# Performance work log

Hardware: AMD Instinct MI355X
Metric: run time of the kernel (lower is better)

The kernel has to match this reference:

```python
import jax, jax.numpy as jnp
import numpy as np

N_NODES = 50000
N_EDGES = 1600000
D = 64  # in_features == out_features (required by residual index_add)
N_NBR_FEA = 41


def setup_inputs() -> dict:
    key = jax.random.key(0)
    k1, k2, k3, k4, k5 = jax.random.split(key, 5)
    return {
        "x": jax.random.normal(k1, (N_NODES, D), dtype=jnp.float32),
        # torch Linear(in=D, out=2D, bias=False): weight shape [2D, D]
        "W": jax.random.normal(k2, (2 * D, D), dtype=jnp.float32) * (1.0 / np.sqrt(D)),
        "edge_sources": jax.random.randint(k3, (N_EDGES,), 0, N_NODES),
        "edge_targets": jax.random.randint(k4, (N_EDGES,), 0, N_NODES),
        # required forward arg; unused when use_distance_nbr=False
        "distance_nbr": jax.random.normal(k5, (N_EDGES, N_NBR_FEA), dtype=jnp.float32),
    }


def reference(x, W, edge_sources, edge_targets, distance_nbr):
    # gather neighbor (target) node features per edge: [E, D]
    h = x[edge_targets]
    # edge linear -> gate + message halves: [E, 2D]
    ge = h @ W.T
    g, e = jnp.split(ge, 2, axis=1)
    msg = jax.nn.sigmoid(g) * e  # gate_activation = Sigmoid(); edge/node activations are None
    # output = input.clone(); output.index_add_(0, edge_sources, g * e)
    return x.at[edge_sources].add(msg)
```

## Files before the change

### kernel.cpp

```cpp
#include <hip/hip_runtime.h>

#define NDIM 64
#define WPAD 68
#define BINSHIFT 8
#define BINSZ 256
#define LCAP 12288
#define EPT 16
#define PCHUNK (256 * EPT)

typedef unsigned short ushort;

__device__ __forceinline__ ushort f2bf(float f) {
    unsigned u = __float_as_uint(f);
    return (ushort)((u + 0x7FFFu + ((u >> 16) & 1u)) >> 16);
}
__device__ __forceinline__ float bflo(unsigned u) { return __uint_as_float(u << 16); }
__device__ __forceinline__ float bfhi(unsigned u) { return __uint_as_float(u & 0xFFFF0000u); }

__global__ __launch_bounds__(256) void node_msg_kernel(
    const float* __restrict__ x, const float* __restrict__ W,
    ushort* __restrict__ Mb, int n_nodes)
{
    __shared__ float sW[128 * WPAD];
    __shared__ float sx[4][4][64];

    for (int i = threadIdx.x; i < 128 * 64; i += 256)
        sW[(i >> 6) * WPAD + (i & 63)] = W[i];
    __syncthreads();

    const int wid  = threadIdx.x >> 6;
    const int lane = threadIdx.x & 63;
    const float4* __restrict__ wg4 = (const float4*)&sW[lane * WPAD];
    const float4* __restrict__ we4 = (const float4*)&sW[(lane + 64) * WPAD];

    int n0 = (blockIdx.x * 4 + wid) * 4;
    int stride = gridDim.x * 16;
    for (; n0 < n_nodes; n0 += stride) {
        #pragma unroll
        for (int q = 0; q < 4; ++q) {
            int n = n0 + q;
            sx[wid][q][lane] = (n < n_nodes) ? x[(size_t)n * NDIM + lane] : 0.0f;
        }
        float g[4] = {0, 0, 0, 0}, e[4] = {0, 0, 0, 0};
        #pragma unroll
        for (int k4 = 0; k4 < 16; ++k4) {
            float4 a = wg4[k4];
            float4 b = we4[k4];
            #pragma unroll
            for (int q = 0; q < 4; ++q) {
                float4 xk = *(const float4*)&sx[wid][q][k4 * 4];
                g[q] = fmaf(xk.x, a.x, g[q]); g[q] = fmaf(xk.y, a.y, g[q]);
                g[q] = fmaf(xk.z, a.z, g[q]); g[q] = fmaf(xk.w, a.w, g[q]);
                e[q] = fmaf(xk.x, b.x, e[q]); e[q] = fmaf(xk.y, b.y, e[q]);
                e[q] = fmaf(xk.z, b.z, e[q]); e[q] = fmaf(xk.w, b.w, e[q]);
            }
        }
        #pragma unroll
        for (int q = 0; q < 4; ++q) {
            int n = n0 + q;
            if (n < n_nodes)
                Mb[(size_t)n * NDIM + lane] = f2bf(e[q] / (1.0f + __expf(-g[q])));
        }
    }
}

__global__ __launch_bounds__(256) void partition_kernel(
    const int* __restrict__ src, const int* __restrict__ tgt,
    int* __restrict__ binCursor, unsigned* __restrict__ binned,
    int n_edges, int nbins)
{
    __shared__ int h[256];
    __shared__ int base[256];
    const int tid = threadIdx.x;

    long long cb = (long long)blockIdx.x * PCHUNK;
    long long cs = (long long)gridDim.x * PCHUNK;
    for (; cb < n_edges; cb += cs) {
        if (tid < nbins) h[tid] = 0;
        __syncthreads();

        unsigned pk[EPT]; ushort ps[EPT]; short pb[EPT];
        #pragma unroll
        for (int r = 0; r < EPT; ++r) {
            long long e = cb + r * 256 + tid;
            pb[r] = -1;
            if (e < n_edges) {
                int s = src[e], t = tgt[e];
                int b = s >> BINSHIFT;
                pk[r] = ((unsigned)(s & (BINSZ - 1)) << 16) | (unsigned)t;
                ps[r] = (ushort)atomicAdd(&h[b], 1);
                pb[r] = (short)b;
            }
        }
        __syncthreads();
        if (tid < nbins) {
            int c = h[tid];
            base[tid] = c ? atomicAdd(&binCursor[tid], c) : 0;
        }
        __syncthreads();
        #pragma unroll
        for (int r = 0; r < EPT; ++r) {
            if (pb[r] >= 0) {
                unsigned d = (unsigned)base[pb[r]] + ps[r];
                if (d < LCAP) binned[(size_t)pb[r] * LCAP + d] = pk[r];
            }
        }
        __syncthreads();
    }
}

__global__ __launch_bounds__(512) void csr_build_kernel(
    const unsigned* __restrict__ binned, const int* __restrict__ binCursor,
    unsigned* __restrict__ node_meta, ushort* __restrict__ entries, int n_nodes)
{
    __shared__ unsigned sE[LCAP];
    __shared__ ushort   sT[LCAP];
    __shared__ int sCnt[BINSZ];
    __shared__ int sOff[BINSZ + 1];
    __shared__ int sCur[BINSZ];

    const int bin = blockIdx.x;
    const int tid = threadIdx.x;
    const int cnt = min(binCursor[bin], LCAP);
    const unsigned* __restrict__ be = &binned[(size_t)bin * LCAP];

    for (int i = tid; i < cnt; i += 512) sE[i] = be[i];
    for (int i = tid; i < BINSZ; i += 512) sCnt[i] = 0;
    for (int i = tid; i < LCAP / 2; i += 512) ((unsigned*)sT)[i] = 0;
    __syncthreads();

    for (int i = tid; i < cnt; i += 512) atomicAdd(&sCnt[sE[i] >> 16], 1);
    __syncthreads();

    if (tid < 64) {
        int c[4]; int s = 0;
        #pragma unroll
        for (int q = 0; q < 4; ++q) { c[q] = (sCnt[tid * 4 + q] + 7) & ~7; s += c[q]; }
        int incl = s;
        #pragma unroll
        for (int d = 1; d < 64; d <<= 1) {
            int t = __shfl_up(incl, d);
            if (tid >= d) incl += t;
        }
        int excl = incl - s;
        #pragma unroll
        for (int q = 0; q < 4; ++q) { sOff[tid * 4 + q] = excl; excl += c[q]; }
        if (tid == 63) sOff[BINSZ] = excl;
    }
    __syncthreads();
    if (tid < BINSZ) sCur[tid] = sOff[tid];
    __syncthreads();

    for (int i = tid; i < cnt; i += 512) {
        unsigned p = sE[i];
        int pos = atomicAdd(&sCur[p >> 16], 1);
        sT[pos] = (ushort)(p & 0xFFFFu);
    }

    const int gbase = bin * LCAP;
    if (tid < BINSZ) {
        int n = (bin << BINSHIFT) + tid;
        if (n < n_nodes) {
            unsigned off = (unsigned)(gbase + sOff[tid]);
            unsigned c   = (unsigned)min(sCnt[tid], 255);
            node_meta[n] = (off << 8) | c;
        }
    }
    __syncthreads();

    const int tot = sOff[BINSZ];
    uint4* __restrict__ dstv = (uint4*)&entries[gbase];
    const uint4* __restrict__ srcv = (const uint4*)sT;
    for (int i = tid; i < tot / 8; i += 512) dstv[i] = srcv[i];
}

__global__ __launch_bounds__(256) void gather_reduce_kernel(
    const float* __restrict__ x, const ushort* __restrict__ Mb,
    const unsigned* __restrict__ node_meta, const ushort* __restrict__ entries,
    float* __restrict__ out, int n_nodes)
{
    const int wid  = threadIdx.x >> 6;
    const int lane = threadIdx.x & 63;
    const int sub  = lane >> 3;
    const int sl   = lane & 7;

    int n = (blockIdx.x * 4 + wid) * 8 + sub;
    bool valid = n < n_nodes;
    int nn = valid ? n : 0;
    unsigned meta = valid ? node_meta[nn] : 0u;
    int cnt = (int)(meta & 255u);
    const ushort* __restrict__ brow = &entries[meta >> 8];

    float acc[8] = {0, 0, 0, 0, 0, 0, 0, 0};
    for (int j = 0; j < cnt; j += 8) {
        uint4 nb = *(const uint4*)&brow[j];
        unsigned id[8] = { nb.x & 0xFFFFu, nb.x >> 16, nb.y & 0xFFFFu, nb.y >> 16,
                           nb.z & 0xFFFFu, nb.z >> 16, nb.w & 0xFFFFu, nb.w >> 16 };
        #pragma unroll
        for (int k = 0; k < 8; ++k) {
            if (j + k < cnt) {
                uint4 v = *(const uint4*)&Mb[(size_t)id[k] * NDIM + sl * 8];
                acc[0] += bflo(v.x); acc[1] += bfhi(v.x);
                acc[2] += bflo(v.y); acc[3] += bfhi(v.y);
                acc[4] += bflo(v.z); acc[5] += bfhi(v.z);
                acc[6] += bflo(v.w); acc[7] += bfhi(v.w);
            }
        }
    }
    if (valid) {
        size_t base = (size_t)n * NDIM + sl * 8;
        float4 x0 = *(const float4*)&x[base];
        float4 x1 = *(const float4*)&x[base + 4];
        float4 o0 = {x0.x + acc[0], x0.y + acc[1], x0.z + acc[2], x0.w + acc[3]};
        float4 o1 = {x1.x + acc[4], x1.y + acc[5], x1.z + acc[6], x1.w + acc[7]};
        *(float4*)&out[base]     = o0;
        *(float4*)&out[base + 4] = o1;
    }
}

__global__ __launch_bounds__(256) void copy_out_kernel(
    const float* __restrict__ x, float* __restrict__ out, size_t n)
{
    size_t i = (size_t)blockIdx.x * 256 + threadIdx.x;
    size_t gs = (size_t)gridDim.x * 256;
    for (; i < n; i += gs) out[i] = x[i];
}

__global__ __launch_bounds__(256) void edge_scatter_kernel(
    const int* __restrict__ src, const int* __restrict__ tgt,
    const ushort* __restrict__ Mb, float* __restrict__ out, int n_edges)
{
    long long total = (long long)n_edges * 16;
    long long i0 = (long long)blockIdx.x * blockDim.x + threadIdx.x;
    long long gs = (long long)gridDim.x * blockDim.x;
    for (long long i = i0; i < total; i += gs) {
        int e = (int)(i >> 4);
        int q = (int)(i & 15);
        int s = src[e];
        int t = tgt[e];
        uint2 v = *(const uint2*)&Mb[(size_t)t * NDIM + q * 4];
        float* o = &out[(size_t)s * NDIM + q * 4];
        atomicAdd(o + 0, bflo(v.x));
        atomicAdd(o + 1, bfhi(v.x));
        atomicAdd(o + 2, bflo(v.y));
        atomicAdd(o + 3, bfhi(v.y));
    }
}

static inline size_t align16(size_t v) { return (v + 15) & ~(size_t)15; }

extern "C" void kernel_launch(void* const* d_in, const int* in_sizes, int n_in,
                              void* d_out, int out_size, void* d_ws, size_t ws_size,
                              hipStream_t stream)
{
    const float* x   = (const float*)d_in[0];
    const float* W   = (const float*)d_in[1];
    const int*   src = (const int*)d_in[2];
    const int*   tgt = (const int*)d_in[3];

    int n_nodes = in_sizes[0] / NDIM;
    int n_edges = in_sizes[2];
    float* out = (float*)d_out;

    int nbins = (n_nodes + BINSZ - 1) >> BINSHIFT;

    char* ws = (char*)d_ws;
    size_t off = 0;
    ushort* Mb = (ushort*)(ws + off);          off = align16(off + (size_t)n_nodes * NDIM * 2);
    unsigned* node_meta = (unsigned*)(ws + off); off = align16(off + (size_t)n_nodes * 4);
    int* binCursor = (int*)(ws + off);         off = align16(off + (size_t)nbins * 4);
    unsigned* binned = (unsigned*)(ws + off);  off = align16(off + (size_t)nbins * LCAP * 4);
    ushort* entries = (ushort*)(ws + off);     off = align16(off + (size_t)nbins * LCAP * 2);
    size_t need = off + 1024;

    int nblocks = (n_nodes + 15) / 16;
    node_msg_kernel<<<nblocks, 256, 0, stream>>>(x, W, Mb, n_nodes);

    if (ws_size >= need && n_nodes <= 65536 && nbins <= 256) {
        hipMemsetAsync(binCursor, 0, (size_t)nbins * sizeof(int), stream);
        int nchunks = (int)(((long long)n_edges + PCHUNK - 1) / PCHUNK);
        partition_kernel<<<nchunks, 256, 0, stream>>>(
            src, tgt, binCursor, binned, n_edges, nbins);
        csr_build_kernel<<<nbins, 512, 0, stream>>>(
            binned, binCursor, node_meta, entries, n_nodes);
        gather_reduce_kernel<<<(n_nodes + 31) / 32, 256, 0, stream>>>(
            x, Mb, node_meta, entries, out, n_nodes);
    } else if (ws_size >= (size_t)n_nodes * NDIM * sizeof(ushort)) {
        copy_out_kernel<<<2048, 256, 0, stream>>>(x, out, (size_t)n_nodes * NDIM);
        long long total = (long long)n_edges * 16;
        edge_scatter_kernel<<<(int)((total + 255) / 256), 256, 0, stream>>>(
            src, tgt, Mb, out, n_edges);
    }
}
```

Baseline: 114.1 us.

## Fuse message and partition kernels; split bf16 messages into column halves for gathering

The node-message GEMV and the edge partition now run as one launch, with blocks split by index between the two jobs. Each can fill idle units while the other runs, and one launch is saved. The bf16 message table is stored as two separate 32-column halves, and the gather runs twice, once per half, so each pass touches a 3.2MB table that fits better in L2. In exchange, the edge list is read twice and there is an extra launch for the second half.

Measured after the change: 118.8 us. +4.1%, slower.

```diff
diff --git a/kernel.cpp b/kernel.cpp
--- a/kernel.cpp
+++ b/kernel.cpp
@@ -7,6 +7,8 @@
 #define LCAP 12288
 #define EPT 16
 #define PCHUNK (256 * EPT)
+#define NMB 512
+#define PB  256
 
 typedef unsigned short ushort;
 
@@ -17,9 +19,9 @@
 __device__ __forceinline__ float bflo(unsigned u) { return __uint_as_float(u << 16); }
 __device__ __forceinline__ float bfhi(unsigned u) { return __uint_as_float(u & 0xFFFF0000u); }
 
-__global__ __launch_bounds__(256) void node_msg_kernel(
+__device__ void node_msg_body(
     const float* __restrict__ x, const float* __restrict__ W,
-    ushort* __restrict__ Mb, int n_nodes)
+    ushort* __restrict__ Mb, int n_nodes, int bid, int nblocks)
 {
     __shared__ float sW[128 * WPAD];
     __shared__ float sx[4][4][64];
@@ -32,9 +34,10 @@
     const int lane = threadIdx.x & 63;
     const float4* __restrict__ wg4 = (const float4*)&sW[lane * WPAD];
     const float4* __restrict__ we4 = (const float4*)&sW[(lane + 64) * WPAD];
-
-    int n0 = (blockIdx.x * 4 + wid) * 4;
-    int stride = gridDim.x * 16;
+    const size_t half_off = (size_t)(lane >> 5) * n_nodes * 32 + (lane & 31);
+
+    int n0 = (bid * 4 + wid) * 4;
+    int stride = nblocks * 16;
     for (; n0 < n_nodes; n0 += stride) {
         #pragma unroll
         for (int q = 0; q < 4; ++q) {
@@ -59,22 +62,22 @@
         for (int q = 0; q < 4; ++q) {
             int n = n0 + q;
             if (n < n_nodes)
-                Mb[(size_t)n * NDIM + lane] = f2bf(e[q] / (1.0f + __expf(-g[q])));
-        }
-    }
-}
-
-__global__ __launch_bounds__(256) void partition_kernel(
+                Mb[half_off + (size_t)n * 32] = f2bf(e[q] / (1.0f + __expf(-g[q])));
+        }
+    }
+}
+
+__device__ void partition_body(
     const int* __restrict__ src, const int* __restrict__ tgt,
     int* __restrict__ binCursor, unsigned* __restrict__ binned,
-    int n_edges, int nbins)
+    int n_edges, int nbins, int bid, int nblocks)
 {
     __shared__ int h[256];
     __shared__ int base[256];
     const int tid = threadIdx.x;
 
-    long long cb = (long long)blockIdx.x * PCHUNK;
-    long long cs = (long long)gridDim.x * PCHUNK;
+    long long cb = (long long)bid * PCHUNK;
+    long long cs = (long long)nblocks * PCHUNK;
     for (; cb < n_edges; cb += cs) {
         if (tid < nbins) h[tid] = 0;
         __syncthreads();
@@ -109,6 +112,19 @@
     }
 }
 
+__global__ __launch_bounds__(256) void fused_msg_partition_kernel(
+    const float* __restrict__ x, const float* __restrict__ W,
+    ushort* __restrict__ Mb, const int* __restrict__ src,
+    const int* __restrict__ tgt, int* __restrict__ binCursor,
+    unsigned* __restrict__ binned, int n_nodes, int n_edges, int nbins)
+{
+    if (blockIdx.x < NMB)
+        node_msg_body(x, W, Mb, n_nodes, blockIdx.x, NMB);
+    else
+        partition_body(src, tgt, binCursor, binned, n_edges, nbins,
+                       blockIdx.x - NMB, PB);
+}
+
 __global__ __launch_bounds__(512) void csr_build_kernel(
     const unsigned* __restrict__ binned, const int* __restrict__ binCursor,
     unsigned* __restrict__ node_meta, ushort* __restrict__ entries, int n_nodes)
@@ -160,11 +176,9 @@
     const int gbase = bin * LCAP;
     if (tid < BINSZ) {
         int n = (bin << BINSHIFT) + tid;
-        if (n < n_nodes) {
-            unsigned off = (unsigned)(gbase + sOff[tid]);
-            unsigned c   = (unsigned)min(sCnt[tid], 255);
-            node_meta[n] = (off << 8) | c;
-        }
+        if (n < n_nodes)
+            node_meta[n] = ((unsigned)(gbase + sOff[tid]) << 8)
+                         | (unsigned)min(sCnt[tid], 255);
     }
     __syncthreads();
 
@@ -174,17 +188,17 @@
     for (int i = tid; i < tot / 8; i += 512) dstv[i] = srcv[i];
 }
 
-__global__ __launch_bounds__(256) void gather_reduce_kernel(
-    const float* __restrict__ x, const ushort* __restrict__ Mb,
+__global__ __launch_bounds__(256) void gather_half_kernel(
+    const float* __restrict__ x, const ushort* __restrict__ Mbh,
     const unsigned* __restrict__ node_meta, const ushort* __restrict__ entries,
-    float* __restrict__ out, int n_nodes)
+    float* __restrict__ out, int n_nodes, int half)
 {
     const int wid  = threadIdx.x >> 6;
     const int lane = threadIdx.x & 63;
-    const int sub  = lane >> 3;
-    const int sl   = lane & 7;
-
-    int n = (blockIdx.x * 4 + wid) * 8 + sub;
+    const int sub  = lane >> 2;
+    const int sl   = lane & 3;
+
+    int n = (blockIdx.x * 4 + wid) * 16 + sub;
     bool valid = n < n_nodes;
     int nn = valid ? n : 0;
     unsigned meta = valid ? node_meta[nn] : 0u;
@@ -199,7 +213,7 @@
         #pragma unroll
         for (int k = 0; k < 8; ++k) {
             if (j + k < cnt) {
-                uint4 v = *(const uint4*)&Mb[(size_t)id[k] * NDIM + sl * 8];
+                uint4 v = *(const uint4*)&Mbh[(size_t)id[k] * 32 + sl * 8];
                 acc[0] += bflo(v.x); acc[1] += bfhi(v.x);
                 acc[2] += bflo(v.y); acc[3] += bfhi(v.y);
                 acc[4] += bflo(v.z); acc[5] += bfhi(v.z);
@@ -208,7 +222,7 @@
         }
     }
     if (valid) {
-        size_t base = (size_t)n * NDIM + sl * 8;
+        size_t base = (size_t)n * NDIM + half * 32 + sl * 8;
         float4 x0 = *(const float4*)&x[base];
         float4 x1 = *(const float4*)&x[base + 4];
         float4 o0 = {x0.x + acc[0], x0.y + acc[1], x0.z + acc[2], x0.w + acc[3]};
@@ -228,7 +242,8 @@
 
 __global__ __launch_bounds__(256) void edge_scatter_kernel(
     const int* __restrict__ src, const int* __restrict__ tgt,
-    const ushort* __restrict__ Mb, float* __restrict__ out, int n_edges)
+    const ushort* __restrict__ Mb, float* __restrict__ out,
+    int n_edges, int n_nodes)
 {
     long long total = (long long)n_edges * 16;
     long long i0 = (long long)blockIdx.x * blockDim.x + threadIdx.x;
@@ -238,7 +253,10 @@
         int q = (int)(i & 15);
         int s = src[e];
         int t = tgt[e];
-        uint2 v = *(const uint2*)&Mb[(size_t)t * NDIM + q * 4];
+        int half = q >> 2;
+        int d    = (q * 4) & 31;
+        uint2 v = *(const uint2*)&Mb[(size_t)half * n_nodes * 32
+                                     + (size_t)t * 32 + d];
         float* o = &out[(size_t)s * NDIM + q * 4];
         atomicAdd(o + 0, bflo(v.x));
         atomicAdd(o + 1, bfhi(v.x));
@@ -266,29 +284,31 @@
 
     char* ws = (char*)d_ws;
     size_t off = 0;
-    ushort* Mb = (ushort*)(ws + off);          off = align16(off + (size_t)n_nodes * NDIM * 2);
+    ushort* Mb = (ushort*)(ws + off);            off = align16(off + (size_t)n_nodes * NDIM * 2);
     unsigned* node_meta = (unsigned*)(ws + off); off = align16(off + (size_t)n_nodes * 4);
-    int* binCursor = (int*)(ws + off);         off = align16(off + (size_t)nbins * 4);
-    unsigned* binned = (unsigned*)(ws + off);  off = align16(off + (size_t)nbins * LCAP * 4);
-    ushort* entries = (ushort*)(ws + off);     off = align16(off + (size_t)nbins * LCAP * 2);
+    int* binCursor = (int*)(ws + off);           off = align16(off + (size_t)nbins * 4);
+    unsigned* binned = (unsigned*)(ws + off);    off = align16(off + (size_t)nbins * LCAP * 4);
+    ushort* entries = (ushort*)(ws + off);       off = align16(off + (size_t)nbins * LCAP * 2);
     size_t need = off + 1024;
-
-    int nblocks = (n_nodes + 15) / 16;
-    node_msg_kernel<<<nblocks, 256, 0, stream>>>(x, W, Mb, n_nodes);
 
     if (ws_size >= need && n_nodes <= 65536 && nbins <= 256) {
         hipMemsetAsync(binCursor, 0, (size_t)nbins * sizeof(int), stream);
-        int nchunks = (int)(((long long)n_edges + PCHUNK - 1) / PCHUNK);
-        partition_kernel<<<nchunks, 256, 0, stream>>>(
-            src, tgt, binCursor, binned, n_edges, nbins);
+        fused_msg_partition_kernel<<<NMB + PB, 256, 0, stream>>>(
+            x, W, Mb, src, tgt, binCursor, binned, n_nodes, n_edges, nbins);
         csr_build_kernel<<<nbins, 512, 0, stream>>>(
             binned, binCursor, node_meta, entries, n_nodes);
-        gather_reduce_kernel<<<(n_nodes + 31) / 32, 256, 0, stream>>>(
-            x, Mb, node_meta, entries, out, n_nodes);
+        int gb = (n_nodes + 63) / 64;
+        gather_half_kernel<<<gb, 256, 0, stream>>>(
+            x, Mb, node_meta, entries, out, n_nodes, 0);
+        gather_half_kernel<<<gb, 256, 0, stream>>>(
+            x, Mb + (size_t)n_nodes * 32, node_meta, entries, out, n_nodes, 1);
     } else if (ws_size >= (size_t)n_nodes * NDIM * sizeof(ushort)) {
+        fused_msg_partition_kernel<<<NMB, 256, 0, stream>>>(
+            x, W, Mb, src, tgt, (int*)nullptr, (unsigned*)nullptr,
+            n_nodes, 0, 0);
         copy_out_kernel<<<2048, 256, 0, stream>>>(x, out, (size_t)n_nodes * NDIM);
         long long total = (long long)n_edges * 16;
         edge_scatter_kernel<<<(int)((total + 255) / 256), 256, 0, stream>>>(
-            src, tgt, Mb, out, n_edges);
-    }
-}
+            src, tgt, Mb, out, n_edges, n_nodes);
+    }
+}
```
